# Performance work log

Measured on AMD Instinct MI355X. Metric: run time of the kernel, lower is better.

The kernel has to match this reference:

```python
import jax, jax.numpy as jnp
import numpy as np

EMBED_DIM = 1024
NUM_HEADS = 16
HEAD_DIM = EMBED_DIM // NUM_HEADS


def setup_inputs() -> dict:
    key = jax.random.key(0)
    k1, k2, k3 = jax.random.split(key, 3)
    B, S = 2, 2048
    x = jax.random.normal(k1, (B, S, EMBED_DIM), dtype=jnp.float32)
    # Xavier-uniform-style init for dense kernels
    lim_qkv = float(np.sqrt(6.0 / (EMBED_DIM + 3 * EMBED_DIM)))
    w_qkv = jax.random.uniform(k2, (EMBED_DIM, 3 * EMBED_DIM), jnp.float32, -lim_qkv, lim_qkv)
    b_qkv = jnp.zeros((3 * EMBED_DIM,), jnp.float32)
    lim_out = float(np.sqrt(6.0 / (EMBED_DIM + EMBED_DIM)))
    w_out = jax.random.uniform(k3, (EMBED_DIM, EMBED_DIM), jnp.float32, -lim_out, lim_out)
    b_out = jnp.zeros((EMBED_DIM,), jnp.float32)
    return {"x": x, "w_qkv": w_qkv, "b_qkv": b_qkv, "w_out": w_out, "b_out": b_out}


def reference(x, w_qkv, b_qkv, w_out, b_out):
    B, S, E = x.shape
    qkv = x @ w_qkv + b_qkv                       # [B, S, 3E]
    qkv = qkv.reshape(B, S, NUM_HEADS, 3 * HEAD_DIM)
    qkv = qkv.transpose(0, 2, 1, 3)               # [B, H, S, 3*dh]
    q, k, v = jnp.split(qkv, 3, axis=-1)          # each [B, H, S, dh]
    scale = 1.0 / jnp.sqrt(jnp.asarray(HEAD_DIM, x.dtype))
    logits = jnp.einsum('bhqd,bhkd->bhqk', q, k) * scale  # [B, H, S, S]
    attn = jax.nn.softmax(logits, axis=-1)
    vals = jnp.einsum('bhqk,bhkd->bhqd', attn, v)  # [B, H, S, dh]
    vals = vals.transpose(0, 2, 1, 3).reshape(B, S, E)
    return vals @ w_out + b_out
```

## Files before the change

kernel.cpp:

```cpp
#include <hip/hip_runtime.h>
#include <cstdint>

typedef unsigned short u16;
typedef unsigned int u32;
typedef __attribute__((ext_vector_type(8))) short bf16x8;
typedef __attribute__((ext_vector_type(4))) float f32x4;

#if __has_builtin(__builtin_amdgcn_exp2f)
#define EXP2(x) __builtin_amdgcn_exp2f(x)
#else
#define EXP2(x) exp2f(x)
#endif

__device__ __forceinline__ u16 f2bf(float f) {
  unsigned u = __float_as_uint(f);
  u += 0x7fffu + ((u >> 16) & 1u);
  return (u16)(u >> 16);
}
__device__ __forceinline__ u32 pk_bf16(float lo, float hi) {
#if __has_builtin(__builtin_amdgcn_cvt_pk_bf16_f32)
  auto r = __builtin_amdgcn_cvt_pk_bf16_f32(lo, hi);
  return __builtin_bit_cast(u32, r);
#else
  u32 a = __float_as_uint(lo), b = __float_as_uint(hi);
  a += 0x7fffu + ((a >> 16) & 1u);
  b += 0x7fffu + ((b >> 16) & 1u);
  return (a >> 16) | (b & 0xffff0000u);
#endif
}

__device__ __forceinline__ void async_load16(const void* g, void* l) {
  typedef const __attribute__((address_space(1))) void* gp_t;
  typedef __attribute__((address_space(3))) void* lp_t;
  __builtin_amdgcn_global_load_lds((gp_t)(uintptr_t)g, (lp_t)(uintptr_t)l, 16, 0, 0);
}

__global__ __launch_bounds__(256) void preprocess(
    const float* __restrict__ x, u16* __restrict__ xb,
    const float* __restrict__ wqkv, u16* __restrict__ dqkv,
    const float* __restrict__ wout, u16* __restrict__ dout)
{
  __shared__ u16 tile[64][65];
  const int t = threadIdx.x;
  const int bx = blockIdx.x;
  if (bx < 2048) {
    const size_t i = ((size_t)bx * 256 + t) * 8;
    const float4 a = *(const float4*)(x + i);
    const float4 b = *(const float4*)(x + i + 4);
    union { u16 u[8]; bf16x8 v; } p;
    p.u[0] = f2bf(a.x); p.u[1] = f2bf(a.y); p.u[2] = f2bf(a.z); p.u[3] = f2bf(a.w);
    p.u[4] = f2bf(b.x); p.u[5] = f2bf(b.y); p.u[6] = f2bf(b.z); p.u[7] = f2bf(b.w);
    *(bf16x8*)(xb + i) = p.v;
    return;
  }
  const int tb = bx - 2048;
  const int bxx = tb & 63, byy = tb >> 6;
  const bool isOut = bxx >= 48;
  const float* src = isOut ? wout : wqkv;
  u16* dst = isOut ? dout : dqkv;
  const int cols = isOut ? 1024 : 3072;
  const int rows = 1024;
  const int tc = (isOut ? (bxx - 48) : bxx) * 64;
  const int tr = byy * 64;
  const int r = t >> 2, c0 = (t & 3) * 16;
  const float* sp = src + (size_t)(tr + r) * cols + tc + c0;
#pragma unroll
  for (int i = 0; i < 16; i += 4) {
    const float4 v = *(const float4*)(sp + i);
    tile[r][c0 + i + 0] = f2bf(v.x);
    tile[r][c0 + i + 1] = f2bf(v.y);
    tile[r][c0 + i + 2] = f2bf(v.z);
    tile[r][c0 + i + 3] = f2bf(v.w);
  }
  __syncthreads();
  u16* dp = dst + (size_t)(tc + r) * rows + tr + c0;
#pragma unroll
  for (int i = 0; i < 16; ++i) dp[i] = tile[c0 + i][r];
}

__global__ __launch_bounds__(256) void gemm_qkv(
    const u16* __restrict__ A, const u16* __restrict__ Bt, const float* __restrict__ bias,
    u16* __restrict__ Qp, u16* __restrict__ Kp, u16* __restrict__ Vtp)
{
  const int Kd = 1024;
  __shared__ __align__(16) u16 As[2][128 * 32];
  __shared__ __align__(16) u16 Bs[2][128 * 32];
  const int t = threadIdx.x;
  const int lane = t & 63, wave = t >> 6;
  const int quad = lane >> 4, m16 = lane & 15;
  const int mb = blockIdx.y * 128, nb = blockIdx.x * 128;
  const int wr = (wave & 1) * 64, wc = (wave >> 1) * 64;

  const int seg = (nb + wc) >> 6;
  const int h = seg / 3;
  const int which = seg - 3 * h;
  const bool isV = (which == 2);

  const int srow = t >> 2;
  const int scol = (t & 3) * 8;
  const u16* Ag0 = A + (size_t)(mb + srow) * Kd + scol;
  const u16* Ag1 = Ag0 + (size_t)64 * Kd;
  const u16* Bg0 = Bt + (size_t)(nb + srow) * Kd + scol;
  const u16* Bg1 = Bg0 + (size_t)64 * Kd;
  const int aoff = t * 8;

  f32x4 acc[4][4] = {};

#define GPRE(k0, B)                                                          \
  do {                                                                       \
    async_load16(Ag0 + (k0), &As[B][aoff]);                                  \
    async_load16(Ag1 + (k0), &As[B][aoff + 2048]);                           \
    async_load16(Bg0 + (k0), &Bs[B][aoff]);                                  \
    async_load16(Bg1 + (k0), &Bs[B][aoff + 2048]);                           \
  } while (0)

#define GSTEP(B)                                                             \
  do {                                                                       \
    bf16x8 af[4], bfr[4];                                                    \
    _Pragma("unroll")                                                        \
    for (int i = 0; i < 4; ++i)                                              \
      af[i] = *(const bf16x8*)(&As[B][(wr + i * 16 + m16) * 32 + quad * 8]); \
    _Pragma("unroll")                                                        \
    for (int i = 0; i < 4; ++i)                                              \
      bfr[i] = *(const bf16x8*)(&Bs[B][(wc + i * 16 + m16) * 32 + quad * 8]); \
    if (isV) {                                                               \
      _Pragma("unroll")                                                      \
      for (int i = 0; i < 4; ++i)                                            \
        _Pragma("unroll")                                                    \
        for (int j = 0; j < 4; ++j)                                          \
          acc[i][j] = __builtin_amdgcn_mfma_f32_16x16x32_bf16(bfr[i], af[j], acc[i][j], 0, 0, 0); \
    } else {                                                                 \
      _Pragma("unroll")                                                      \
      for (int i = 0; i < 4; ++i)                                            \
        _Pragma("unroll")                                                    \
        for (int j = 0; j < 4; ++j)                                          \
          acc[i][j] = __builtin_amdgcn_mfma_f32_16x16x32_bf16(af[i], bfr[j], acc[i][j], 0, 0, 0); \
    }                                                                        \
  } while (0)

  GPRE(0, 0);
  __syncthreads();
  for (int k0 = 0; k0 < Kd; k0 += 64) {
    GPRE(k0 + 32, 1);
    GSTEP(0);
    __syncthreads();
    if (k0 + 64 < Kd) GPRE(k0 + 64, 0);
    GSTEP(1);
    __syncthreads();
  }
#undef GPRE
#undef GSTEP

  const int b = mb >> 11;
  const size_t bh64 = (size_t)((b << 4) | h);

  if (isV) {
    const int sIbase = (mb & 2047) + wr;
    u16* dstV = Vtp + bh64 * 64 * 2048;
#pragma unroll
    for (int i = 0; i < 4; ++i)
#pragma unroll
      for (int r = 0; r < 4; ++r) {
        const int d = i * 16 + quad * 4 + r;
        const float bv = bias[nb + wc + d];
        u16* rp = dstV + (size_t)d * 2048 + sIbase;
#pragma unroll
        for (int j = 0; j < 4; ++j)
          rp[j * 16 + m16] = f2bf(acc[i][j][r] + bv);
      }
  } else {
    u16* dstP = (which == 0) ? Qp : Kp;
    const float qs = (which == 0) ? 0.18033688011112042f : 1.0f;
#pragma unroll
    for (int j = 0; j < 4; ++j) {
      const int base = nb + wc + j * 16;
      const float bv = bias[base + m16];
      const int d = (base & 63) + m16;
#pragma unroll
      for (int i = 0; i < 4; ++i)
#pragma unroll
        for (int r = 0; r < 4; ++r) {
          const int row = mb + wr + i * 16 + quad * 4 + r;
          const int sI = row & 2047;
          dstP[(bh64 * 2048 + sI) * 64 + d] = f2bf((acc[i][j][r] + bv) * qs);
        }
    }
  }
}

__global__ __launch_bounds__(256) void gemm_out(
    const u16* __restrict__ A, const u16* __restrict__ Bt, const float* __restrict__ bias,
    float* __restrict__ Outp)
{
  const int Kd = 1024;
  __shared__ __align__(16) u16 As[2][64 * 32];
  __shared__ __align__(16) u16 Bs[2][128 * 32];
  const int t = threadIdx.x;
  const int lane = t & 63, wave = t >> 6;
  const int quad = lane >> 4, m16 = lane & 15;
  const int mb = blockIdx.y * 64, nb = blockIdx.x * 128;
  const int wr = (wave & 1) * 32, wc = (wave >> 1) * 64;

  const int srow = t >> 2;
  const int scol = (t & 3) * 8;
  const u16* Ag0 = A + (size_t)(mb + srow) * Kd + scol;
  const u16* Bg0 = Bt + (size_t)(nb + srow) * Kd + scol;
  const u16* Bg1 = Bg0 + (size_t)64 * Kd;
  const int aoff = t * 8;

  f32x4 acc[2][4] = {};

#define OPRE(k0, B)                                                          \
  do {                                                                       \
    async_load16(Ag0 + (k0), &As[B][aoff]);                                  \
    async_load16(Bg0 + (k0), &Bs[B][aoff]);                                  \
    async_load16(Bg1 + (k0), &Bs[B][aoff + 2048]);                           \
  } while (0)

#define OSTEP(B)                                                             \
  do {                                                                       \
    bf16x8 af[2], bfr[4];                                                    \
    _Pragma("unroll")                                                        \
    for (int i = 0; i < 2; ++i)                                              \
      af[i] = *(const bf16x8*)(&As[B][(wr + i * 16 + m16) * 32 + quad * 8]); \
    _Pragma("unroll")                                                        \
    for (int j = 0; j < 4; ++j)                                              \
      bfr[j] = *(const bf16x8*)(&Bs[B][(wc + j * 16 + m16) * 32 + quad * 8]); \
    _Pragma("unroll")                                                        \
    for (int i = 0; i < 2; ++i)                                              \
      _Pragma("unroll")                                                      \
      for (int j = 0; j < 4; ++j)                                            \
        acc[i][j] = __builtin_amdgcn_mfma_f32_16x16x32_bf16(af[i], bfr[j], acc[i][j], 0, 0, 0); \
  } while (0)

  OPRE(0, 0);
  __syncthreads();
  for (int k0 = 0; k0 < Kd; k0 += 64) {
    OPRE(k0 + 32, 1);
    OSTEP(0);
    __syncthreads();
    if (k0 + 64 < Kd) OPRE(k0 + 64, 0);
    OSTEP(1);
    __syncthreads();
  }
#undef OPRE
#undef OSTEP

#pragma unroll
  for (int j = 0; j < 4; ++j) {
    const int col = nb + wc + j * 16 + m16;
    const float bv = bias[col];
#pragma unroll
    for (int i = 0; i < 2; ++i)
#pragma unroll
      for (int r = 0; r < 4; ++r) {
        const int row = mb + wr + i * 16 + quad * 4 + r;
        Outp[(size_t)row * 1024 + col] = acc[i][j][r] + bv;
      }
  }
}

__global__ __launch_bounds__(256) void flash_attn(
    const u16* __restrict__ Q, const u16* __restrict__ K, const u16* __restrict__ Vt,
    u16* __restrict__ O)
{
  const int S = 2048;
  __shared__ __align__(16) u16 Kl[2][64 * 64];
  __shared__ __align__(16) u16 Vl[2][64 * 64];
  __shared__ __align__(16) u32 Pl[4][2][16 * 32];
  const int t = threadIdx.x;
  const int lane = t & 63, w = t >> 6;
  const int quad = lane >> 4, m16 = lane & 15;

  const int f = blockIdx.x;
  const int wi = f >> 3;
  const int bh = (f & 7) + 8 * (wi & 3);
  const int q0 = (wi >> 2) * 128;

  const u16* Qb = Q + (size_t)bh * S * 64;
  const u16* Kb = K + (size_t)bh * S * 64;
  const u16* Vb = Vt + (size_t)bh * 64 * S;

  bf16x8 qf[2][2];
#pragma unroll
  for (int g = 0; g < 2; ++g)
#pragma unroll
    for (int ks = 0; ks < 2; ++ks)
      qf[g][ks] = *(const bf16x8*)(Qb + (size_t)(q0 + w * 32 + g * 16 + m16) * 64 + ks * 32 + quad * 8);

  const u16* Kg[2]; const u16* Vg[2]; int soff[2];
#pragma unroll
  for (int l = 0; l < 2; ++l) {
    const int idx = l * 256 + t;
    const int row = idx >> 3, slot = idx & 7;
    const int sg = slot ^ (row & 7);
    Kg[l] = Kb + row * 64 + sg * 8;
    Vg[l] = Vb + (size_t)row * S + sg * 8;
    soff[l] = idx * 8;
  }

  f32x4 ot[2][4] = {};
  f32x4 lr4[2] = {{0.f,0.f,0.f,0.f},{0.f,0.f,0.f,0.f}};
  u32* const Pw0 = &Pl[w][0][0];
  u32* const Pw1 = &Pl[w][1][0];

#define PREFETCH(kvp, B)                                                     \
  do {                                                                       \
    _Pragma("unroll")                                                        \
    for (int l = 0; l < 2; ++l) async_load16(Kg[l] + (kvp) * 64, &Kl[B][soff[l]]); \
    _Pragma("unroll")                                                        \
    for (int l = 0; l < 2; ++l) async_load16(Vg[l] + (kvp), &Vl[B][soff[l]]);      \
  } while (0)

#define STEP(B)                                                              \
  do {                                                                       \
    f32x4 st[2][4] = {};                                                     \
    _Pragma("unroll")                                                        \
    for (int nt = 0; nt < 4; ++nt) {                                         \
      const int j = nt * 16 + m16;                                           \
      const u16* rowp = &Kl[B][j * 64];                                      \
      const bf16x8 kb0 = *(const bf16x8*)(rowp + ((quad ^ (j & 7)) * 8));    \
      const bf16x8 kb1 = *(const bf16x8*)(rowp + (((4 + quad) ^ (j & 7)) * 8)); \
      st[0][nt] = __builtin_amdgcn_mfma_f32_16x16x32_bf16(kb0, qf[0][0], st[0][nt], 0, 0, 0); \
      st[1][nt] = __builtin_amdgcn_mfma_f32_16x16x32_bf16(kb0, qf[1][0], st[1][nt], 0, 0, 0); \
      st[0][nt] = __builtin_amdgcn_mfma_f32_16x16x32_bf16(kb1, qf[0][1], st[0][nt], 0, 0, 0); \
      st[1][nt] = __builtin_amdgcn_mfma_f32_16x16x32_bf16(kb1, qf[1][1], st[1][nt], 0, 0, 0); \
    }                                                                        \
    _Pragma("unroll")                                                        \
    for (int g = 0; g < 2; ++g) {                                            \
      u32* const Pw = g ? Pw1 : Pw0;                                         \
      _Pragma("unroll")                                                      \
      for (int nt = 0; nt < 4; ++nt) {                                       \
        f32x4 p;                                                             \
        _Pragma("unroll")                                                    \
        for (int r = 0; r < 4; ++r) p[r] = EXP2(st[g][nt][r]);               \
        lr4[g] += p;                                                         \
        const u32 lo = pk_bf16(p[0], p[1]);                                  \
        const u32 hi = pk_bf16(p[2], p[3]);                                  \
        const int gp = (2 * nt + (quad >> 1)) ^ (m16 & 7);                   \
        u32* dst = Pw + m16 * 32 + gp * 4 + (quad & 1) * 2;                  \
        *(uint2*)dst = make_uint2(lo, hi);                                   \
      }                                                                      \
    }                                                                        \
    _Pragma("unroll")                                                        \
    for (int ks = 0; ks < 2; ++ks) {                                         \
      const int pg = (ks * 4 + quad) ^ (m16 & 7);                            \
      const bf16x8 pb0 = *(const bf16x8*)(Pw0 + m16 * 32 + pg * 4);          \
      const bf16x8 pb1 = *(const bf16x8*)(Pw1 + m16 * 32 + pg * 4);          \
      _Pragma("unroll")                                                      \
      for (int dt = 0; dt < 4; ++dt) {                                       \
        const int d = dt * 16 + m16;                                         \
        const bf16x8 va = *(const bf16x8*)(&Vl[B][d * 64] + (((ks * 4 + quad) ^ (d & 7)) * 8)); \
        ot[0][dt] = __builtin_amdgcn_mfma_f32_16x16x32_bf16(va, pb0, ot[0][dt], 0, 0, 0); \
        ot[1][dt] = __builtin_amdgcn_mfma_f32_16x16x32_bf16(va, pb1, ot[1][dt], 0, 0, 0); \
      }                                                                      \
    }                                                                        \
  } while (0)

  PREFETCH(0, 0);
  __syncthreads();

  for (int kv0 = 0; kv0 < S; kv0 += 128) {
    PREFETCH(kv0 + 64, 1);
    STEP(0);
    __syncthreads();
    if (kv0 + 128 < S) PREFETCH(kv0 + 128, 0);
    STEP(1);
    __syncthreads();
  }
#undef PREFETCH
#undef STEP

  const int b = bh >> 4, h = bh & 15;
#pragma unroll
  for (int g = 0; g < 2; ++g) {
    float l = lr4[g][0] + lr4[g][1] + lr4[g][2] + lr4[g][3];
    l += __shfl_xor(l, 16, 64);
    l += __shfl_xor(l, 32, 64);
    const float inv = 1.0f / l;
    const int q = q0 + w * 32 + g * 16 + m16;
    u16* base = O + ((size_t)b * 2048 + q) * 1024 + h * 64;
#pragma unroll
    for (int dt = 0; dt < 4; ++dt) {
      const u32 lo = pk_bf16(ot[g][dt][0] * inv, ot[g][dt][1] * inv);
      const u32 hi = pk_bf16(ot[g][dt][2] * inv, ot[g][dt][3] * inv);
      *(uint2*)(base + dt * 16 + quad * 4) = make_uint2(lo, hi);
    }
  }
}

extern "C" void kernel_launch(void* const* d_in, const int* in_sizes, int n_in,
                              void* d_out, int out_size, void* d_ws, size_t ws_size,
                              hipStream_t stream)
{
  const float* x     = (const float*)d_in[0];
  const float* w_qkv = (const float*)d_in[1];
  const float* b_qkv = (const float*)d_in[2];
  const float* w_out = (const float*)d_in[3];
  const float* b_out = (const float*)d_in[4];
  float* out = (float*)d_out;

  u16* ws     = (u16*)d_ws;
  u16* xb     = ws;
  u16* WtQKV  = xb + 4194304;
  u16* WtOut  = WtQKV + 3145728;
  u16* Qm     = WtOut + 1048576;
  u16* Km     = Qm + 4194304;
  u16* Vtm    = Km + 4194304;
  u16* AO     = Vtm + 4194304;

  preprocess<<<3072, 256, 0, stream>>>(x, xb, w_qkv, WtQKV, w_out, WtOut);
  gemm_qkv<<<dim3(24, 32), 256, 0, stream>>>(xb, WtQKV, b_qkv, Qm, Km, Vtm);
  flash_attn<<<512, 256, 0, stream>>>(Qm, Km, Vtm, AO);
  gemm_out<<<dim3(8, 64), 256, 0, stream>>>(AO, WtOut, b_out, out);
}
```

Before: 189.9 us.

## Switch attention to 32x32x16 MFMA and pass P through registers via permlane32 swap

The flash attention inner step now uses 32x32x16 bf16 MFMA tiles instead of 16x16x32 for both QK^T and PV. The softmax probabilities are repacked between the score and PV operand layouts with a permlane32 swap, so they no longer take a round trip through LDS. This removes the per-wave P shared buffer along with its stores and loads, and halves the number of MFMA issues. In exchange it adds 16-wide accumulators, which raise register pressure, and a fallback path built on shuffles for toolchains without the builtin.

```diff
diff --git a/kernel.cpp b/kernel.cpp
--- a/kernel.cpp
+++ b/kernel.cpp
@@ -5,6 +5,8 @@
 typedef unsigned int u32;
 typedef __attribute__((ext_vector_type(8))) short bf16x8;
 typedef __attribute__((ext_vector_type(4))) float f32x4;
+typedef __attribute__((ext_vector_type(16))) float f32x16;
+typedef __attribute__((ext_vector_type(2))) unsigned int u32x2;
 
 #if __has_builtin(__builtin_amdgcn_exp2f)
 #define EXP2(x) __builtin_amdgcn_exp2f(x)
@@ -26,6 +28,19 @@
   a += 0x7fffu + ((a >> 16) & 1u);
   b += 0x7fffu + ((b >> 16) & 1u);
   return (a >> 16) | (b & 0xffff0000u);
+#endif
+}
+
+__device__ __forceinline__ void plane32swap(u32 x, u32 y, u32& r0, u32& r1) {
+#if __has_builtin(__builtin_amdgcn_permlane32_swap)
+  u32x2 r = __builtin_amdgcn_permlane32_swap(x, y, false, false);
+  r0 = r[0]; r1 = r[1];
+#else
+  const u32 xs = (u32)__shfl_xor((int)x, 32, 64);
+  const u32 ys = (u32)__shfl_xor((int)y, 32, 64);
+  const bool hi = (threadIdx.x & 32) != 0;
+  r0 = hi ? ys : x;
+  r1 = hi ? y : xs;
 #endif
 }
 
@@ -267,10 +282,9 @@
   const int S = 2048;
   __shared__ __align__(16) u16 Kl[2][64 * 64];
   __shared__ __align__(16) u16 Vl[2][64 * 64];
-  __shared__ __align__(16) u32 Pl[4][2][16 * 32];
   const int t = threadIdx.x;
   const int lane = t & 63, w = t >> 6;
-  const int quad = lane >> 4, m16 = lane & 15;
+  const int l31 = lane & 31, hi = lane >> 5;
 
   const int f = blockIdx.x;
   const int wi = f >> 3;
@@ -281,12 +295,10 @@
   const u16* Kb = K + (size_t)bh * S * 64;
   const u16* Vb = Vt + (size_t)bh * 64 * S;
 
-  bf16x8 qf[2][2];
-#pragma unroll
-  for (int g = 0; g < 2; ++g)
-#pragma unroll
-    for (int ks = 0; ks < 2; ++ks)
-      qf[g][ks] = *(const bf16x8*)(Qb + (size_t)(q0 + w * 32 + g * 16 + m16) * 64 + ks * 32 + quad * 8);
+  bf16x8 qf[4];
+#pragma unroll
+  for (int dc = 0; dc < 4; ++dc)
+    qf[dc] = *(const bf16x8*)(Qb + (size_t)(q0 + w * 32 + l31) * 64 + dc * 16 + hi * 8);
 
   const u16* Kg[2]; const u16* Vg[2]; int soff[2];
 #pragma unroll
@@ -299,10 +311,8 @@
     soff[l] = idx * 8;
   }
 
-  f32x4 ot[2][4] = {};
-  f32x4 lr4[2] = {{0.f,0.f,0.f,0.f},{0.f,0.f,0.f,0.f}};
-  u32* const Pw0 = &Pl[w][0][0];
-  u32* const Pw1 = &Pl[w][1][0];
+  f32x16 ot[2] = {};
+  float lr4[4] = {0.f, 0.f, 0.f, 0.f};
 
 #define PREFETCH(kvp, B)                                                     \
   do {                                                                       \
@@ -314,45 +324,42 @@
 
 #define STEP(B)                                                              \
   do {                                                                       \
-    f32x4 st[2][4] = {};                                                     \
-    _Pragma("unroll")                                                        \
-    for (int nt = 0; nt < 4; ++nt) {                                         \
-      const int j = nt * 16 + m16;                                           \
-      const u16* rowp = &Kl[B][j * 64];                                      \
-      const bf16x8 kb0 = *(const bf16x8*)(rowp + ((quad ^ (j & 7)) * 8));    \
-      const bf16x8 kb1 = *(const bf16x8*)(rowp + (((4 + quad) ^ (j & 7)) * 8)); \
-      st[0][nt] = __builtin_amdgcn_mfma_f32_16x16x32_bf16(kb0, qf[0][0], st[0][nt], 0, 0, 0); \
-      st[1][nt] = __builtin_amdgcn_mfma_f32_16x16x32_bf16(kb0, qf[1][0], st[1][nt], 0, 0, 0); \
-      st[0][nt] = __builtin_amdgcn_mfma_f32_16x16x32_bf16(kb1, qf[0][1], st[0][nt], 0, 0, 0); \
-      st[1][nt] = __builtin_amdgcn_mfma_f32_16x16x32_bf16(kb1, qf[1][1], st[1][nt], 0, 0, 0); \
-    }                                                                        \
-    _Pragma("unroll")                                                        \
-    for (int g = 0; g < 2; ++g) {                                            \
-      u32* const Pw = g ? Pw1 : Pw0;                                         \
-      _Pragma("unroll")                                                      \
-      for (int nt = 0; nt < 4; ++nt) {                                       \
-        f32x4 p;                                                             \
+    bf16x8 pa[4];                                                            \
+    _Pragma("unroll")                                                        \
+    for (int kt = 0; kt < 2; ++kt) {                                         \
+      f32x16 st = {0.f,0.f,0.f,0.f, 0.f,0.f,0.f,0.f,                         \
+                   0.f,0.f,0.f,0.f, 0.f,0.f,0.f,0.f};                        \
+      const int kvr = kt * 32 + l31;                                         \
+      const u16* krow = &Kl[B][kvr * 64];                                    \
+      _Pragma("unroll")                                                      \
+      for (int dc = 0; dc < 4; ++dc) {                                       \
+        const bf16x8 kb = *(const bf16x8*)(krow + (((dc * 2 + hi) ^ (kvr & 7)) * 8)); \
+        st = __builtin_amdgcn_mfma_f32_32x32x16_bf16(kb, qf[dc], st, 0, 0, 0); \
+      }                                                                      \
+      float p[16];                                                           \
+      _Pragma("unroll")                                                      \
+      for (int r = 0; r < 16; ++r) { p[r] = EXP2(st[r]); lr4[r & 3] += p[r]; } \
+      _Pragma("unroll")                                                      \
+      for (int cc = 0; cc < 2; ++cc) {                                       \
+        union { u32 u[4]; bf16x8 v; } fr;                                    \
         _Pragma("unroll")                                                    \
-        for (int r = 0; r < 4; ++r) p[r] = EXP2(st[g][nt][r]);               \
-        lr4[g] += p;                                                         \
-        const u32 lo = pk_bf16(p[0], p[1]);                                  \
-        const u32 hi = pk_bf16(p[2], p[3]);                                  \
-        const int gp = (2 * nt + (quad >> 1)) ^ (m16 & 7);                   \
-        u32* dst = Pw + m16 * 32 + gp * 4 + (quad & 1) * 2;                  \
-        *(uint2*)dst = make_uint2(lo, hi);                                   \
+        for (int i = 0; i < 2; ++i) {                                        \
+          const u32 xx = pk_bf16(p[8 * cc + 2 * i + 0], p[8 * cc + 2 * i + 1]); \
+          const u32 yy = pk_bf16(p[8 * cc + 2 * i + 4], p[8 * cc + 2 * i + 5]); \
+          u32 r0, r1;                                                        \
+          plane32swap(xx, yy, r0, r1);                                       \
+          fr.u[i] = r0; fr.u[2 + i] = r1;                                    \
+        }                                                                    \
+        pa[kt * 2 + cc] = fr.v;                                              \
       }                                                                      \
     }                                                                        \
     _Pragma("unroll")                                                        \
-    for (int ks = 0; ks < 2; ++ks) {                                         \
-      const int pg = (ks * 4 + quad) ^ (m16 & 7);                            \
-      const bf16x8 pb0 = *(const bf16x8*)(Pw0 + m16 * 32 + pg * 4);          \
-      const bf16x8 pb1 = *(const bf16x8*)(Pw1 + m16 * 32 + pg * 4);          \
-      _Pragma("unroll")                                                      \
-      for (int dt = 0; dt < 4; ++dt) {                                       \
-        const int d = dt * 16 + m16;                                         \
-        const bf16x8 va = *(const bf16x8*)(&Vl[B][d * 64] + (((ks * 4 + quad) ^ (d & 7)) * 8)); \
-        ot[0][dt] = __builtin_amdgcn_mfma_f32_16x16x32_bf16(va, pb0, ot[0][dt], 0, 0, 0); \
-        ot[1][dt] = __builtin_amdgcn_mfma_f32_16x16x32_bf16(va, pb1, ot[1][dt], 0, 0, 0); \
+    for (int c = 0; c < 4; ++c) {                                            \
+      _Pragma("unroll")                                                      \
+      for (int dt = 0; dt < 2; ++dt) {                                       \
+        const int dr = dt * 32 + l31;                                        \
+        const bf16x8 va = *(const bf16x8*)(&Vl[B][dr * 64] + (((c * 2 + hi) ^ (dr & 7)) * 8)); \
+        ot[dt] = __builtin_amdgcn_mfma_f32_32x32x16_bf16(va, pa[c], ot[dt], 0, 0, 0); \
       }                                                                      \
     }                                                                        \
   } while (0)
@@ -371,22 +378,20 @@
 #undef PREFETCH
 #undef STEP
 
+  float l = lr4[0] + lr4[1] + lr4[2] + lr4[3];
+  l += __shfl_xor(l, 32, 64);
+  const float inv = 1.0f / l;
   const int b = bh >> 4, h = bh & 15;
-#pragma unroll
-  for (int g = 0; g < 2; ++g) {
-    float l = lr4[g][0] + lr4[g][1] + lr4[g][2] + lr4[g][3];
-    l += __shfl_xor(l, 16, 64);
-    l += __shfl_xor(l, 32, 64);
-    const float inv = 1.0f / l;
-    const int q = q0 + w * 32 + g * 16 + m16;
-    u16* base = O + ((size_t)b * 2048 + q) * 1024 + h * 64;
-#pragma unroll
-    for (int dt = 0; dt < 4; ++dt) {
-      const u32 lo = pk_bf16(ot[g][dt][0] * inv, ot[g][dt][1] * inv);
-      const u32 hi = pk_bf16(ot[g][dt][2] * inv, ot[g][dt][3] * inv);
-      *(uint2*)(base + dt * 16 + quad * 4) = make_uint2(lo, hi);
+  const int q = q0 + w * 32 + l31;
+  u16* base = O + ((size_t)b * 2048 + q) * 1024 + h * 64;
+#pragma unroll
+  for (int dt = 0; dt < 2; ++dt)
+#pragma unroll
+    for (int g4 = 0; g4 < 4; ++g4) {
+      const u32 lo = pk_bf16(ot[dt][4 * g4 + 0] * inv, ot[dt][4 * g4 + 1] * inv);
+      const u32 h2 = pk_bf16(ot[dt][4 * g4 + 2] * inv, ot[dt][4 * g4 + 3] * inv);
+      *(uint2*)(base + dt * 32 + 8 * g4 + 4 * hi) = make_uint2(lo, h2);
     }
-  }
 }
 
 extern "C" void kernel_launch(void* const* d_in, const int* in_sizes, int n_in,
```

Measured after the change: 188.2 us. No clear change (-0.9%).
